# Optimization experiments

Measured on AMD Instinct MI355X. Metric: run time of the kernel, lower is better.

The kernel has to match this reference:

```python
import jax, jax.numpy as jnp
import numpy as np

N, E = 40000, 640000
D, H, DK = 128, 8, 16   # out_dim, n_heads, d_k = D // H
T, R = 3, 4             # num node types, num relation types


def setup_inputs() -> dict:
    key = jax.random.key(0)
    ks = jax.random.split(key, 16)
    glorot = lambda k, shape, fan: jax.random.normal(k, shape, jnp.float32) * np.sqrt(2.0 / fan)
    inp = {
        'node_inp': jax.random.normal(ks[0], (N, D), jnp.float32),
        'node_type': jax.random.randint(ks[1], (N,), 0, T),
        'edge_index': jax.random.randint(ks[2], (2, E), 0, N),
        'edge_type': jax.random.randint(ks[3], (E,), 0, R),
        'node_position': jax.random.randint(ks[4], (N,), 0, N),
        # per-node-type Linear weights, stored [T, in, out] (y = x @ W + b)
        'Kw': glorot(ks[5], (T, D, D), 2 * D), 'Kb': jnp.zeros((T, D), jnp.float32),
        'Qw': glorot(ks[6], (T, D, D), 2 * D), 'Qb': jnp.zeros((T, D), jnp.float32),
        'Vw': glorot(ks[7], (T, D, D), 2 * D), 'Vb': jnp.zeros((T, D), jnp.float32),
        'Aw': glorot(ks[8], (T, D, D), 2 * D), 'Ab': jnp.zeros((T, D), jnp.float32),
        'relation_pri': jnp.ones((T, R, T, H), jnp.float32),
        'relation_att': glorot(ks[9], (R, H, DK, DK), 2 * DK),
        'relation_msg': glorot(ks[10], (R, H, DK, DK), 2 * DK),
        'relation_s2u': glorot(ks[11], (D, D), 2 * D),
        'skip': jnp.ones((T,), jnp.float32),
    }
    return inp


def reference(node_inp, node_type, edge_index, edge_type, node_position,
              Kw, Kb, Qw, Qb, Vw, Vb, Aw, Ab,
              relation_pri, relation_att, relation_msg, relation_s2u, skip):
    n = node_inp.shape[0]
    src, tgt = edge_index[0], edge_index[1]  # j (source), i (target)
    ar = jnp.arange(n)

    # per-type K/Q/V projections for every node: [T, N, D], then select own type
    k_all = jnp.einsum('nd,tdo->tno', node_inp, Kw) + Kb[:, None, :]
    q_all = jnp.einsum('nd,tdo->tno', node_inp, Qw) + Qb[:, None, :]
    v_all = jnp.einsum('nd,tdo->tno', node_inp, Vw) + Vb[:, None, :]
    k_node = k_all[node_type, ar]
    q_node = q_all[node_type, ar]
    v_node = v_all[node_type, ar]

    k_j = k_node[src].reshape(-1, H, DK)
    v_j = v_node[src].reshape(-1, H, DK)
    q_i = q_node[tgt].reshape(-1, H, DK)

    # per-relation attention / message transforms (select per edge relation)
    k_t = jnp.zeros_like(k_j)
    v_t = jnp.zeros_like(v_j)
    for r in range(R):
        sel = (edge_type == r)[:, None, None]
        k_t = jnp.where(sel, jnp.einsum('ehd,hdf->ehf', k_j, relation_att[r]), k_t)
        v_t = jnp.where(sel, jnp.einsum('ehd,hdf->ehf', v_j, relation_msg[r]), v_t)

    st, tt = node_type[src], node_type[tgt]
    pri = relation_pri[tt, edge_type, st]                       # [E, H]
    att_raw = (q_i * k_t).sum(-1) * pri / np.sqrt(DK)           # [E, H]

    # scatter-softmax over edges sharing the same target node
    m = jax.ops.segment_max(att_raw, tgt, num_segments=n)
    m = jnp.where(jnp.isfinite(m), m, 0.0)
    ex = jnp.exp(att_raw - m[tgt])
    den = jax.ops.segment_sum(ex, tgt, num_segments=n)
    att = ex / (den[tgt] + 1e-16)

    msg = (v_t * att[:, :, None]).reshape(-1, D)
    aggr = jax.ops.segment_sum(msg, tgt, num_segments=n)        # scatter-add

    # speaker information: edges with edge_type==0, message from target rep to source index
    sp_in = v_all[1][tgt]                                       # v_linears[1](node_inp[edge_index_i])
    sp_msg = sp_in @ relation_s2u                               # [E, D]
    drop_idx = jnp.where(edge_type == 0, src, n)                # out-of-range -> dropped
    speaker_info = jnp.zeros((n, D), node_inp.dtype).at[drop_idx].set(sp_msg, mode='drop')

    aggr = jax.nn.gelu(aggr + speaker_info, approximate=False)

    # target-specific aggregation with per-type learnable skip (dropout=eval identity)
    a_all = jnp.einsum('no,tof->tnf', aggr, Aw) + Ab[:, None, :]
    a_node = a_all[node_type, ar]
    alpha = jax.nn.sigmoid(skip)[node_type][:, None]
    return a_node * alpha + node_inp * (1.0 - alpha)
```

## Files before the change

### kernel.cpp

```cpp
#include <hip/hip_runtime.h>
#include <hip/hip_bf16.h>
#include <math.h>

#define ND 128
#define NH 8
#define DKK 16
#define NT 3
#define NR 4
#define NB 8
#define NMAT 12
#define SCB 4096

typedef unsigned short ushort_t;
typedef __bf16 bf16_t;
typedef bf16_t bf16x8 __attribute__((ext_vector_type(8)));
typedef float f32x4 __attribute__((ext_vector_type(4)));

__device__ __forceinline__ float bf2f(unsigned short u) {
    union { unsigned int i; float f; } v; v.i = ((unsigned int)u) << 16; return v.f;
}
__device__ __forceinline__ unsigned short f2bf(float f) {
    union { float f; unsigned int i; } v; v.f = f;
    unsigned int x = v.i;
    unsigned int lsb = (x >> 16) & 1u;
    x += 0x7fffu + lsb;
    return (unsigned short)(x >> 16);
}
__device__ __forceinline__ unsigned int pk2(float a, float b) {
    return (unsigned int)f2bf(a) | ((unsigned int)f2bf(b) << 16);
}
__device__ __forceinline__ void load_bf8(const ushort_t* p, float* o) {
    uint4 u = *reinterpret_cast<const uint4*>(p);
    o[0]=bf2f(u.x & 0xffff); o[1]=bf2f(u.x >> 16);
    o[2]=bf2f(u.y & 0xffff); o[3]=bf2f(u.y >> 16);
    o[4]=bf2f(u.z & 0xffff); o[5]=bf2f(u.z >> 16);
    o[6]=bf2f(u.w & 0xffff); o[7]=bf2f(u.w >> 16);
}
__device__ __forceinline__ bf16x8 as_bf16x8(uint4 u) {
    union { uint4 u; bf16x8 v; } c; c.u = u; return c.v;
}


__global__ void k_zero(int n, int* offs, int* winner, int* tcnt) {
    int i = blockIdx.x * 256 + threadIdx.x;
    if (i < n) { offs[i] = 0; winner[i] = -1; }
    if (i < NT) tcnt[i] = 0;
}

__global__ void k_count(int n, int e, const int* src, const int* tgt, const int* etype,
                        const int* ntype, int* offs, int* winner, int* tcnt, int* rank) {
    int i = blockIdx.x * 256 + threadIdx.x;
    if (i < e) {
        rank[i] = atomicAdd(&offs[tgt[i]], 1);
        if (etype[i] == 0) atomicMax(&winner[src[i]], i);
    }
    if (i < n) {
        int t = ntype[i];
        int lane = threadIdx.x & 63;
        #pragma unroll
        for (int tt = 0; tt < NT; tt++) {
            bool me = (t == tt);
            unsigned long long m = __ballot(me);
            if (me) {
                int lower = __popcll(m & ((1ull << lane) - 1ull));
                if (lower == 0) atomicAdd(&tcnt[tt], __popcll(m));
            }
        }
    }
}


__global__ void k_scanA(int n, const int* offs, int* bsum) {
    __shared__ int red[256];
    int b = blockIdx.x, tid = threadIdx.x;
    int base = b * SCB + tid * 16;
    int s = 0;
    #pragma unroll
    for (int i = 0; i < 16; i++) {
        int idx = base + i;
        if (idx < n) s += offs[idx];
    }
    red[tid] = s;
    __syncthreads();
    for (int d = 128; d > 0; d >>= 1) {
        if (tid < d) red[tid] += red[tid + d];
        __syncthreads();
    }
    if (tid == 0) bsum[b] = red[0];
}

__global__ void k_scanB(int nb, const int* bsum, int* boff,
                        const int* tcnt, int* tnext, int* tstart) {
    if (threadIdx.x == 0) {
        int run = 0;
        for (int b = 0; b < nb; b++) { boff[b] = run; run += bsum[b]; }
        int t0 = 0;
        for (int t = 0; t < NT; t++) { tnext[t] = t0; tstart[t] = t0; t0 += tcnt[t]; }
    }
}

__global__ void k_scanC(int n, int* offs, const int* boff) {
    __shared__ int red[256];
    int b = blockIdx.x, tid = threadIdx.x;
    int base = b * SCB + tid * 16;
    int v[16];
    int s = 0;
    #pragma unroll
    for (int i = 0; i < 16; i++) {
        int idx = base + i;
        v[i] = (idx < n) ? offs[idx] : 0;
        s += v[i];
    }
    red[tid] = s;
    __syncthreads();
    for (int d = 1; d < 256; d <<= 1) {
        int vv = (tid >= d) ? red[tid - d] : 0;
        __syncthreads();
        red[tid] += vv;
        __syncthreads();
    }
    int run = boff[b] + red[tid] - s;
    #pragma unroll
    for (int i = 0; i < 16; i++) {
        int idx = base + i;
        if (idx < n) { offs[idx] = run; run += v[i]; }
    }
    if (base <= n && n < base + 16) offs[n] = run;
}

__global__ void k_scatter(int n, int e, const int* src, const int* tgt, const int* etype,
                          const int* ntype, const int* offs, const int* rank,
                          int* eord, int mode, int* tnext, int* order) {
    int i = blockIdx.x * 256 + threadIdx.x;
    if (i < e) {
        int p = offs[tgt[i]] + rank[i];
        if (mode) {
            int s = src[i];
            eord[p] = (s * NR + etype[i]) | (ntype[s] << 28);
        } else {
            eord[p] = i;
        }
    }
    if (i < n) {
        int t = ntype[i];
        int lane = threadIdx.x & 63;
        #pragma unroll
        for (int tt = 0; tt < NT; tt++) {
            bool me = (t == tt);
            unsigned long long m = __ballot(me);
            if (me) {
                int lower = __popcll(m & ((1ull << lane) - 1ull));
                int leader = __ffsll((long long)m) - 1;
                int base = 0;
                if (lane == leader) base = atomicAdd(&tnext[tt], __popcll(m));
                base = __shfl(base, leader, 64);
                order[base + lower] = i;
            }
        }
    }
}


__global__ void k_pack(const float* Qw, const float* Qb, const float* Kw, const float* Kb,
                       const float* Vw, const float* Vb, const float* Aw, const float* Ab,
                       const float* s2u, const float* r_att, const float* r_msg,
                       ushort_t* Wall, float* bcat) {
    int blk = blockIdx.x;
    int kb = blk & 3;
    int c = (blk >> 2) & 7;
    int tm = blk >> 5;
    int m = tm % NMAT, t = tm / NMAT;
    int lane = threadIdx.x;
    int nn = c * 16 + (lane & 15);
    int quad = lane >> 4;
    int k0 = kb * 32 + quad * 8;
    ushort_t* dst = Wall + (size_t)blk * 512 + lane * 8;

    if (m == 0 || m == 5 || m == 10 || m == 11) {
        const float* W; const float* B;
        if (m == 0)       { W = Qw + (size_t)t * ND * ND; B = Qb + t * ND; }
        else if (m == 5)  { W = Vw + (size_t)ND * ND;     B = Vb + ND; }
        else if (m == 10) { W = Aw + (size_t)t * ND * ND; B = Ab + t * ND; }
        else              { W = s2u;                      B = nullptr; }
        #pragma unroll
        for (int j = 0; j < 8; j++) dst[j] = f2bf(W[(size_t)(k0 + j) * ND + nn]);
        if (kb == 0 && quad == 0)
            bcat[(t * NMAT + m) * ND + nn] = B ? B[nn] : 0.f;
    } else {
        int r = (m <= 4) ? (m - 1) : (m - 6);
        const float* W0 = (m <= 4) ? Kw : Vw;
        const float* B0 = (m <= 4) ? Kb : Vb;
        const float* Wr = (m <= 4) ? r_att : r_msg;
        int h = c, f = lane & 15;
        float wcol[16];
        #pragma unroll
        for (int jj = 0; jj < 16; jj++)
            wcol[jj] = Wr[(((size_t)r * NH + h) * DKK + jj) * DKK + f];
        #pragma unroll
        for (int j = 0; j < 8; j++) {
            const float* row = W0 + ((size_t)t * ND + (k0 + j)) * ND + h * DKK;
            float s = 0.f;
            #pragma unroll
            for (int jj = 0; jj < 16; jj++) s += row[jj] * wcol[jj];
            dst[j] = f2bf(s);
        }
        if (kb == 0 && quad == 0) {
            const float* brow = B0 + t * ND + h * DKK;
            float sb = 0.f;
            #pragma unroll
            for (int jj = 0; jj < 16; jj++) sb += brow[jj] * wcol[jj];
            bcat[(t * NMAT + m) * ND + nn] = sb;
        }
    }
}

__global__ void __launch_bounds__(256) k_projm(
    int n, const float* x_in, const int* order,
    const int* tcnt, const int* tstart,
    const ushort_t* Wall, const float* bcat,
    int m0, int nm,
    ushort_t* out_qn, ushort_t* out_kt, ushort_t* out_v1, ushort_t* out_vt)
{
    __shared__ __align__(16) ushort_t xs[4096];
    __shared__ int nodes[32];
    int b = blockIdx.x;
    int nb0 = (tcnt[0] + 31) >> 5, nb1 = (tcnt[1] + 31) >> 5, nb2 = (tcnt[2] + 31) >> 5;
    int t, lb;
    if (b < nb0)                  { t = 0; lb = b; }
    else if (b < nb0 + nb1)       { t = 1; lb = b - nb0; }
    else if (b < nb0 + nb1 + nb2) { t = 2; lb = b - nb0 - nb1; }
    else return;
    int segoff = lb * 32;
    int cnt = min(32, tcnt[t] - segoff);
    int segbase = tstart[t] + segoff;
    int tid = threadIdx.x;
    if (tid < 32) nodes[tid] = (tid < cnt) ? order[segbase + tid] : -1;
    __syncthreads();
    {
        int row = tid >> 3;
        int d0 = (tid & 7) * 16;
        int rt = row >> 4, rl = row & 15;
        int kb = d0 >> 5, q0 = (d0 >> 3) & 3;
        uint4 c0, c1;
        if (row < cnt) {
            const float4* xp4 = (const float4*)(x_in + (size_t)nodes[row] * ND + d0);
            float4 a = xp4[0], b2 = xp4[1], c2 = xp4[2], d4 = xp4[3];
            c0.x = pk2(a.x, a.y);   c0.y = pk2(a.z, a.w);
            c0.z = pk2(b2.x, b2.y); c0.w = pk2(b2.z, b2.w);
            c1.x = pk2(c2.x, c2.y); c1.y = pk2(c2.z, c2.w);
            c1.z = pk2(d4.x, d4.y); c1.w = pk2(d4.z, d4.w);
        } else {
            c0.x = c0.y = c0.z = c0.w = 0u;
            c1 = c0;
        }
        *(uint4*)&xs[((rt * 4 + kb) * 64 + q0 * 16 + rl) * 8]       = c0;
        *(uint4*)&xs[((rt * 4 + kb) * 64 + (q0 + 1) * 16 + rl) * 8] = c1;
    }
    __syncthreads();

    int w = tid >> 6, lane = tid & 63;
    int rt = w & 1;
    bf16x8 afr[4];
    #pragma unroll
    for (int kb = 0; kb < 4; kb++)
        afr[kb] = as_bf16x8(*(const uint4*)&xs[((rt * 4 + kb) * 64 + lane) * 8]);
    int nct = nm * 8;
    for (int ct = (w >> 1); ct < nct; ct += 2) {
        int m = m0 + (ct >> 3), c = ct & 7;
        const uint4* bp = (const uint4*)(Wall + ((((size_t)t * NMAT + m) * 8 + c) * 4) * 512);
        f32x4 acc = {0.f, 0.f, 0.f, 0.f};
        #pragma unroll
        for (int kb = 0; kb < 4; kb++) {
            bf16x8 bfr = as_bf16x8(bp[kb * 64 + lane]);
            acc = __builtin_amdgcn_mfma_f32_16x16x32_bf16(afr[kb], bfr, acc, 0, 0, 0);
        }
        int col = c * 16 + (lane & 15);
        float bias = bcat[(t * NMAT + m) * ND + col];
        int rbase = rt * 16 + (lane >> 4) * 4;
        #pragma unroll
        for (int r = 0; r < 4; r++) {
            int grow = rbase + r;
            if (grow >= cnt) continue;
            int node = nodes[grow];
            ushort_t val = f2bf(acc[r] + bias);
            if (m == 0)       out_qn[(size_t)node * ND + col] = val;
            else if (m <= 4)  out_kt[((size_t)node * NR + (m - 1)) * ND + col] = val;
            else if (m == 5)  out_v1[(size_t)node * ND + col] = val;
            else              out_vt[((size_t)node * NR + (m - 6)) * ND + col] = val;
        }
    }
}

__global__ void __launch_bounds__(256) k_sfinal(
    int n, const float* x_in, const int* order, const int* tcnt, const int* tstart,
    const int* winner, const int* tgt, const ushort_t* v1b,
    const ushort_t* Wall, const float* bcat, const float* skip,
    const float* aggr, float* out)
{
    __shared__ __align__(16) float xf[32 * 132];
    __shared__ __align__(16) ushort_t xs[4096];
    __shared__ int nodes[32];
    __shared__ int wsrc[32];
    int b = blockIdx.x;
    int nb0 = (tcnt[0] + 31) >> 5, nb1 = (tcnt[1] + 31) >> 5, nb2 = (tcnt[2] + 31) >> 5;
    int t, lb;
    if (b < nb0)                  { t = 0; lb = b; }
    else if (b < nb0 + nb1)       { t = 1; lb = b - nb0; }
    else if (b < nb0 + nb1 + nb2) { t = 2; lb = b - nb0 - nb1; }
    else return;
    int segoff = lb * 32;
    int cnt = min(32, tcnt[t] - segoff);
    int segbase = tstart[t] + segoff;
    int tid = threadIdx.x;
    if (tid < 32) {
        int nd = (tid < cnt) ? order[segbase + tid] : -1;
        nodes[tid] = nd;
        int wi = (nd >= 0) ? winner[nd] : -1;
        wsrc[tid] = (wi >= 0) ? tgt[wi] : -1;
    }
    __syncthreads();
    {
        int row = tid >> 3;
        int d0 = (tid & 7) * 16;
        int rt = row >> 4, rl = row & 15;
        int kb = d0 >> 5, q0 = (d0 >> 3) & 3;
        uint4 c0, c1;
        int s = (row < cnt) ? wsrc[row] : -1;
        if (s >= 0) {
            const uint4* vp = (const uint4*)(v1b + (size_t)s * ND + d0);
            c0 = vp[0]; c1 = vp[1];
        } else { c0.x = c0.y = c0.z = c0.w = 0u; c1 = c0; }
        *(uint4*)&xs[((rt * 4 + kb) * 64 + q0 * 16 + rl) * 8]       = c0;
        *(uint4*)&xs[((rt * 4 + kb) * 64 + (q0 + 1) * 16 + rl) * 8] = c1;
    }
    __syncthreads();
    int w = tid >> 6, lane = tid & 63;
    int rt = w & 1;
    {
        bf16x8 afr[4];
        #pragma unroll
        for (int kb = 0; kb < 4; kb++)
            afr[kb] = as_bf16x8(*(const uint4*)&xs[((rt * 4 + kb) * 64 + lane) * 8]);
        for (int ct = (w >> 1); ct < 8; ct += 2) {
            const uint4* bp = (const uint4*)(Wall + (((size_t)11 * 8 + ct) * 4) * 512);
            f32x4 acc = {0.f, 0.f, 0.f, 0.f};
            #pragma unroll
            for (int kb = 0; kb < 4; kb++) {
                bf16x8 bfr = as_bf16x8(bp[kb * 64 + lane]);
                acc = __builtin_amdgcn_mfma_f32_16x16x32_bf16(afr[kb], bfr, acc, 0, 0, 0);
            }
            int col = ct * 16 + (lane & 15);
            int rbase = rt * 16 + (lane >> 4) * 4;
            #pragma unroll
            for (int r = 0; r < 4; r++) {
                int grow = rbase + r;
                if (grow >= cnt) continue;
                int node = nodes[grow];
                float g = aggr[(size_t)node * ND + col] + acc[r];
                g = 0.5f * g * (1.f + erff(g * 0.70710678118f));
                xf[grow * 132 + col] = g;
            }
        }
    }
    __syncthreads();
    {
        int row = tid >> 3;
        int d0 = (tid & 7) * 16;
        int rt2 = row >> 4, rl = row & 15;
        int kb = d0 >> 5, q0 = (d0 >> 3) & 3;
        uint4 c0, c1;
        if (row < cnt) {
            const float4* xp4 = (const float4*)(xf + row * 132 + d0);
            float4 a = xp4[0], b2 = xp4[1], c2 = xp4[2], d4 = xp4[3];
            c0.x = pk2(a.x, a.y);   c0.y = pk2(a.z, a.w);
            c0.z = pk2(b2.x, b2.y); c0.w = pk2(b2.z, b2.w);
            c1.x = pk2(c2.x, c2.y); c1.y = pk2(c2.z, c2.w);
            c1.z = pk2(d4.x, d4.y); c1.w = pk2(d4.z, d4.w);
        } else {
            c0.x = c0.y = c0.z = c0.w = 0u;
            c1 = c0;
        }
        *(uint4*)&xs[((rt2 * 4 + kb) * 64 + q0 * 16 + rl) * 8]       = c0;
        *(uint4*)&xs[((rt2 * 4 + kb) * 64 + (q0 + 1) * 16 + rl) * 8] = c1;
    }
    __syncthreads();
    float alpha = 1.f / (1.f + expf(-skip[t]));
    {
        bf16x8 afr[4];
        #pragma unroll
        for (int kb = 0; kb < 4; kb++)
            afr[kb] = as_bf16x8(*(const uint4*)&xs[((rt * 4 + kb) * 64 + lane) * 8]);
        for (int ct = (w >> 1); ct < 8; ct += 2) {
            const uint4* bp = (const uint4*)(Wall + ((((size_t)t * NMAT + 10) * 8 + ct) * 4) * 512);
            f32x4 acc = {0.f, 0.f, 0.f, 0.f};
            #pragma unroll
            for (int kb = 0; kb < 4; kb++) {
                bf16x8 bfr = as_bf16x8(bp[kb * 64 + lane]);
                acc = __builtin_amdgcn_mfma_f32_16x16x32_bf16(afr[kb], bfr, acc, 0, 0, 0);
            }
            int col = ct * 16 + (lane & 15);
            float bias = bcat[(t * NMAT + 10) * ND + col];
            int rbase = rt * 16 + (lane >> 4) * 4;
            #pragma unroll
            for (int r = 0; r < 4; r++) {
                int grow = rbase + r;
                if (grow >= cnt) continue;
                int node = nodes[grow];
                float xin = x_in[(size_t)node * ND + col];
                out[(size_t)node * ND + col] = (acc[r] + bias) * alpha + xin * (1.f - alpha);
            }
        }
    }
}

__global__ void __launch_bounds__(256) k_attmd(
    int n, const int* off, const int* srp, const int* ntype,
    const ushort_t* qn, const ushort_t* kt, const float* r_pri,
    float* atts, ushort_t* mb, float* db)
{
    int wv = threadIdx.x >> 6, lane = threadIdx.x & 63;
    int i = blockIdx.x * 4 + wv;
    if (i >= n) return;
    int h = lane & 7, slot = lane >> 3;
    int tt = ntype[i];
    float qf[16];
    load_bf8(qn + (size_t)i * ND + h * DKK, qf);
    load_bf8(qn + (size_t)i * ND + h * DKK + 8, qf + 8);
    const float* prib = r_pri + (size_t)(tt * NR * NT) * NH + h;
    int d0 = off[i], d1 = off[i + 1];
    float m = -3.0e38f, den = 0.f;
    #pragma unroll 2
    for (int p0 = d0; p0 < d1; p0 += 8) {
        int p = p0 + slot;
        bool live = (p < d1);
        int sp = live ? srp[p] : 0;
        int sr = sp & 0x0fffffff;
        int st = ((unsigned int)sp) >> 28;
        int r = sr & (NR - 1);
        float kf[16];
        const ushort_t* kp = kt + (size_t)sr * ND + h * DKK;
        load_bf8(kp, kf);
        load_bf8(kp + 8, kf + 8);
        float a = 0.f;
        #pragma unroll
        for (int f = 0; f < 16; f++) a += qf[f] * kf[f];
        float pri = prib[(r * NT + st) * NH];
        float logit = fminf(fmaxf(a * pri * 0.25f, -1.0e4f), 1.0e4f);
        if (live) {
            atts[(size_t)p * NH + h] = logit;
            float mnew = fmaxf(m, logit);
            den = den * expf(m - mnew) + expf(logit - mnew);
            m = mnew;
        }
    }
    #pragma unroll
    for (int d = 8; d < 64; d <<= 1) {
        float mo = __shfl_xor(m, d, 64);
        float dn = __shfl_xor(den, d, 64);
        float mnew = fmaxf(m, mo);
        den = den * expf(m - mnew) + dn * expf(mo - mnew);
        m = mnew;
    }
    if (slot == 0) {
        ushort_t mh = (d1 > d0) ? f2bf(m) : (ushort_t)0;
        float dfin = (d1 > d0) ? den * expf(m - bf2f(mh)) : 0.f;
        mb[i * NH + h] = mh;
        db[i * NH + h] = dfin;
    }
}

__global__ void __launch_bounds__(256) k_aggr_fast(
    int n, const int* off, const int* srp, const ushort_t* vt, const float* atts,
    const ushort_t* mb, const float* db, float* aggr)
{
    int wv = threadIdx.x >> 6, lane = threadIdx.x & 63;
    int i = blockIdx.x * 4 + wv;
    if (i >= n) return;
    int h = lane >> 3;
    float mref = bf2f(mb[i * NH + h]);
    float inv = 1.f / (db[i * NH + h] + 1e-16f);
    int d0 = off[i], d1 = off[i + 1];
    float acc0 = 0.f, acc1 = 0.f;
    #pragma unroll 4
    for (int p = d0; p < d1; p++) {
        int sr = srp[p] & 0x0fffffff;
        float w = expf(atts[(size_t)p * NH + h] - mref) * inv;
        unsigned int u = *reinterpret_cast<const unsigned int*>(
            vt + (size_t)sr * ND + lane * 2);
        acc0 += w * bf2f(u & 0xffff);
        acc1 += w * bf2f(u >> 16);
    }
    float2 o; o.x = acc0; o.y = acc1;
    *reinterpret_cast<float2*>(aggr + (size_t)i * ND + lane * 2) = o;
}


__global__ void k_proj(int n, const float* x_in, const int* ntype, const int* order,
                       const float* Kw, const float* Kb,
                       const float* Qw, const float* Qb,
                       const float* Vw, const float* Vb,
                       ushort_t* kn, ushort_t* qn, ushort_t* vn, ushort_t* v1) {
    __shared__ float xs[NB][ND];
    __shared__ int nodes[NB];
    __shared__ int types[NB];
    int tid = threadIdx.x;
    int base = blockIdx.x * NB;
    int cnt = min(NB, n - base);
    if (tid < cnt) { int nd = order[base + tid]; nodes[tid] = nd; types[tid] = ntype[nd]; }
    __syncthreads();
    for (int j = 0; j < cnt; j++) xs[j][tid] = x_in[(size_t)nodes[j] * ND + tid];
    __syncthreads();
    bool uni = (types[0] == types[cnt - 1]);
    for (int m = 0; m < 4; m++) {
        const float *W, *B; ushort_t* out; int forced_t = -1;
        if (m == 0)      { W = Kw; B = Kb; out = kn; }
        else if (m == 1) { W = Qw; B = Qb; out = qn; }
        else if (m == 2) { W = Vw; B = Vb; out = vn; }
        else             { W = Vw; B = Vb; out = v1; forced_t = 1; }
        if (uni || forced_t >= 0) {
            int t = (forced_t >= 0) ? forced_t : types[0];
            float bias = B[t * ND + tid];
            float acc[NB];
            #pragma unroll
            for (int j = 0; j < NB; j++) acc[j] = bias;
            const float* Wp = W + (size_t)t * ND * ND + tid;
            for (int d = 0; d < ND; d++) {
                float w = Wp[(size_t)d * ND];
                #pragma unroll
                for (int j = 0; j < NB; j++) acc[j] += xs[j][d] * w;
            }
            for (int j = 0; j < cnt; j++) out[(size_t)nodes[j] * ND + tid] = f2bf(acc[j]);
        } else {
            for (int j = 0; j < cnt; j++) {
                int t = types[j];
                float acc = B[t * ND + tid];
                const float* Wp = W + (size_t)t * ND * ND + tid;
                for (int d = 0; d < ND; d++) acc += xs[j][d] * Wp[(size_t)d * ND];
                out[(size_t)nodes[j] * ND + tid] = f2bf(acc);
            }
        }
    }
}

__global__ void k_att(int e, const int* src, const int* tgt, const int* etype, const int* ntype,
                      const ushort_t* kn, const ushort_t* qn,
                      const float* r_att, const float* r_pri, float* att) {
    int id = blockIdx.x * 256 + threadIdx.x;
    if (id >= e * NH) return;
    int ee = id >> 3, h = id & 7;
    int s = src[ee], t = tgt[ee], r = etype[ee];
    float kf[16], qf[16];
    load_bf8(kn + (size_t)s * ND + h * DKK, kf);
    load_bf8(kn + (size_t)s * ND + h * DKK + 8, kf + 8);
    load_bf8(qn + (size_t)t * ND + h * DKK, qf);
    load_bf8(qn + (size_t)t * ND + h * DKK + 8, qf + 8);
    const float* W = r_att + (size_t)(r * NH + h) * DKK * DKK;
    float kt[16];
    #pragma unroll
    for (int f = 0; f < 16; f++) kt[f] = 0.f;
    #pragma unroll 4
    for (int d = 0; d < 16; d++) {
        float kd = kf[d];
        #pragma unroll
        for (int f = 0; f < 16; f++) kt[f] += kd * W[d * 16 + f];
    }
    float a = 0.f;
    #pragma unroll
    for (int f = 0; f < 16; f++) a += qf[f] * kt[f];
    int tt = ntype[t], st = ntype[s];
    float pri = r_pri[((tt * NR + r) * NT + st) * NH + h];
    float logit = a * pri * 0.25f;
    logit = fminf(fmaxf(logit, -1.0e4f), 1.0e4f);
    att[(size_t)ee * NH + h] = logit;
}

__global__ void k_mden(int n, const int* off, const int* sorted,
                       const float* att, ushort_t* mb, float* db) {
    int id = blockIdx.x * 256 + threadIdx.x;
    if (id >= n * NH) return;
    int i = id >> 3, h = id & 7;
    int d0 = off[i], d1 = off[i + 1];
    float m = -3.0e38f;
    for (int p = d0; p < d1; p++) m = fmaxf(m, att[(size_t)sorted[p] * NH + h]);
    ushort_t mh = (d1 > d0) ? f2bf(m) : (ushort_t)0;
    float mref = bf2f(mh);
    float den = 0.f;
    for (int p = d0; p < d1; p++) den += expf(att[(size_t)sorted[p] * NH + h] - mref);
    mb[id] = mh;
    db[id] = den;
}

__global__ void k_norm(int e, const int* tgt, const ushort_t* mb, const float* db, float* att) {
    int id = blockIdx.x * 256 + threadIdx.x;
    if (id >= e * NH) return;
    int ee = id >> 3, h = id & 7;
    int t = tgt[ee];
    float w = expf(att[id] - bf2f(mb[t * NH + h])) / (db[t * NH + h] + 1e-16f);
    att[id] = w;
}

__global__ void k_aggr(int n, const int* off, const int* sorted, const int* src, const int* etype,
                       const ushort_t* vn, const float* r_msg, const float* att, float* aggr) {
    int wv = threadIdx.x >> 6, lane = threadIdx.x & 63;
    int i = blockIdx.x * 4 + wv;
    if (i >= n) return;
    int h = lane >> 3, f0 = (lane & 7) * 2;
    int d0 = off[i], d1 = off[i + 1];
    float acc0 = 0.f, acc1 = 0.f;
    for (int p = d0; p < d1; p++) {
        int ee = sorted[p];
        int s = src[ee], r = etype[ee];
        float w = att[(size_t)ee * NH + h];
        float vj[16];
        load_bf8(vn + (size_t)s * ND + h * DKK, vj);
        load_bf8(vn + (size_t)s * ND + h * DKK + 8, vj + 8);
        const float* Wm = r_msg + (size_t)(r * NH + h) * DKK * DKK + f0;
        float a0 = 0.f, a1 = 0.f;
        #pragma unroll
        for (int d = 0; d < 16; d++) {
            a0 += vj[d] * Wm[d * 16];
            a1 += vj[d] * Wm[d * 16 + 1];
        }
        acc0 += w * a0; acc1 += w * a1;
    }
    aggr[(size_t)i * ND + h * DKK + f0]     = acc0;
    aggr[(size_t)i * ND + h * DKK + f0 + 1] = acc1;
}

__global__ void k_spk(int n, const int* winner, const int* tgt, const ushort_t* v1,
                      const float* s2u, float* aggr) {
    __shared__ float xs[NB][ND];
    __shared__ int wn[NB];
    int tid = threadIdx.x;
    int base = blockIdx.x * NB;
    int cnt = min(NB, n - base);
    if (tid < cnt) wn[tid] = winner[base + tid];
    __syncthreads();
    for (int j = 0; j < cnt; j++) {
        int w = wn[j];
        xs[j][tid] = (w >= 0) ? bf2f(v1[(size_t)tgt[w] * ND + tid]) : 0.f;
    }
    __syncthreads();
    float acc[NB];
    #pragma unroll
    for (int j = 0; j < NB; j++) acc[j] = 0.f;
    const float* Wp = s2u + tid;
    for (int d = 0; d < ND; d++) {
        float w = Wp[(size_t)d * ND];
        #pragma unroll
        for (int j = 0; j < NB; j++) acc[j] += xs[j][d] * w;
    }
    for (int j = 0; j < cnt; j++) {
        size_t idx = (size_t)(base + j) * ND + tid;
        float g = aggr[idx] + acc[j];
        g = 0.5f * g * (1.f + erff(g * 0.70710678118f));
        aggr[idx] = g;
    }
}

__global__ void k_final(int n, const float* x_in, const int* ntype, const int* order,
                        const float* Aw, const float* Ab, const float* skip,
                        const float* aggr, float* out) {
    __shared__ float xs[NB][ND];
    __shared__ int nodes[NB];
    __shared__ int types[NB];
    int tid = threadIdx.x;
    int base = blockIdx.x * NB;
    int cnt = min(NB, n - base);
    if (tid < cnt) { int nd = order[base + tid]; nodes[tid] = nd; types[tid] = ntype[nd]; }
    __syncthreads();
    for (int j = 0; j < cnt; j++) xs[j][tid] = aggr[(size_t)nodes[j] * ND + tid];
    __syncthreads();
    bool uni = (types[0] == types[cnt - 1]);
    if (uni) {
        int t = types[0];
        float bias = Ab[t * ND + tid];
        float acc[NB];
        #pragma unroll
        for (int j = 0; j < NB; j++) acc[j] = bias;
        const float* Wp = Aw + (size_t)t * ND * ND + tid;
        for (int d = 0; d < ND; d++) {
            float w = Wp[(size_t)d * ND];
            #pragma unroll
            for (int j = 0; j < NB; j++) acc[j] += xs[j][d] * w;
        }
        float alpha = 1.f / (1.f + expf(-skip[t]));
        for (int j = 0; j < cnt; j++) {
            float xin = x_in[(size_t)nodes[j] * ND + tid];
            out[(size_t)nodes[j] * ND + tid] = acc[j] * alpha + xin * (1.f - alpha);
        }
    } else {
        for (int j = 0; j < cnt; j++) {
            int t = types[j];
            float acc = Ab[t * ND + tid];
            const float* Wp = Aw + (size_t)t * ND * ND + tid;
            for (int d = 0; d < ND; d++) acc += xs[j][d] * Wp[(size_t)d * ND];
            float alpha = 1.f / (1.f + expf(-skip[t]));
            float xin = x_in[(size_t)nodes[j] * ND + tid];
            out[(size_t)nodes[j] * ND + tid] = acc * alpha + xin * (1.f - alpha);
        }
    }
}

extern "C" void kernel_launch(void* const* d_in, const int* in_sizes, int n_in,
                              void* d_out, int out_size, void* d_ws, size_t ws_size,
                              hipStream_t stream) {
    const float* node_inp = (const float*)d_in[0];
    const int* node_type  = (const int*)d_in[1];
    const int* edge_index = (const int*)d_in[2];
    const int* edge_type  = (const int*)d_in[3];
    const float* Kw = (const float*)d_in[5];
    const float* Kb = (const float*)d_in[6];
    const float* Qw = (const float*)d_in[7];
    const float* Qb = (const float*)d_in[8];
    const float* Vw = (const float*)d_in[9];
    const float* Vb = (const float*)d_in[10];
    const float* Aw = (const float*)d_in[11];
    const float* Ab = (const float*)d_in[12];
    const float* r_pri = (const float*)d_in[13];
    const float* r_att = (const float*)d_in[14];
    const float* r_msg = (const float*)d_in[15];
    const float* s2u   = (const float*)d_in[16];
    const float* skip  = (const float*)d_in[17];

    int n = in_sizes[1];
    int e = in_sizes[3];
    const int* srcp = edge_index;
    const int* tgtp = edge_index + e;

    char* wsp = (char*)d_ws;
    size_t woff = 0;
    auto alloc = [&](size_t b) { void* p = wsp + woff; woff += (b + 255) & ~(size_t)255; return p; };

    int* offs     = (int*)alloc((size_t)(n + 1) * 4);
    int* winner   = (int*)alloc((size_t)n * 4);
    int* order    = (int*)alloc((size_t)n * 4);
    int* tcnt     = (int*)alloc(16);
    int* tnext    = (int*)alloc(16);
    int* tstart   = (int*)alloc(16);
    int* bsum     = (int*)alloc(4096);
    int* boff     = (int*)alloc(4096);
    int* eord     = (int*)alloc((size_t)e * 4);
    ushort_t* mb  = (ushort_t*)alloc((size_t)n * NH * 2);
    float* db     = (float*)alloc((size_t)n * NH * 4);
    ushort_t* v1b = (ushort_t*)alloc((size_t)n * ND * 2);
    float* att    = (float*)alloc((size_t)e * NH * 4);
    size_t commonEnd = woff;

    int* rank = (int*)att;

    ushort_t* Wall  = (ushort_t*)alloc((size_t)NT * NMAT * 8 * 4 * 512 * 2);
    float* bcat     = (float*)alloc((size_t)NT * NMAT * ND * 4);
    char* F         = (char*)alloc((size_t)n * 1536);
    size_t fastEnd = woff;

    int gn = (n + 255) / 256;
    int ge = (e + 255) / 256;
    int nbscan = n / SCB + 1;
    int fast = (ws_size >= fastEnd) ? 1 : 0;

    k_zero<<<gn, 256, 0, stream>>>(n, offs, winner, tcnt);
    k_count<<<ge, 256, 0, stream>>>(n, e, srcp, tgtp, edge_type, node_type, offs, winner, tcnt, rank);
    k_scanA<<<nbscan, 256, 0, stream>>>(n, offs, bsum);
    k_scanB<<<1, 64, 0, stream>>>(nbscan, bsum, boff, tcnt, tnext, tstart);
    k_scanC<<<nbscan, 256, 0, stream>>>(n, offs, boff);
    k_scatter<<<ge, 256, 0, stream>>>(n, e, srcp, tgtp, edge_type, node_type, offs, rank,
                                      eord, fast, tnext, order);

    if (fast) {
        ushort_t* qn  = (ushort_t*)F;
        ushort_t* kt  = (ushort_t*)(F + (size_t)n * 256);
        ushort_t* vt  = (ushort_t*)F;
        float* aggr   = (float*)(F + (size_t)n * 1024);
        int gproj = (n + 31) / 32 + NT;

        k_pack<<<NT * NMAT * 8 * 4, 64, 0, stream>>>(Qw, Qb, Kw, Kb, Vw, Vb, Aw, Ab,
                                                     s2u, r_att, r_msg, Wall, bcat);
        k_projm<<<gproj, 256, 0, stream>>>(n, node_inp, order, tcnt, tstart, Wall, bcat,
                                           0, 6, qn, kt, v1b, (ushort_t*)nullptr);
        k_attmd<<<(n + 3) / 4, 256, 0, stream>>>(n, offs, eord, node_type,
                                                 qn, kt, r_pri, att, mb, db);
        k_projm<<<gproj, 256, 0, stream>>>(n, node_inp, order, tcnt, tstart, Wall, bcat,
                                           6, 4, (ushort_t*)nullptr, (ushort_t*)nullptr,
                                           (ushort_t*)nullptr, vt);
        k_aggr_fast<<<(n + 3) / 4, 256, 0, stream>>>(n, offs, eord, vt, att, mb, db, aggr);
        k_sfinal<<<gproj, 256, 0, stream>>>(n, node_inp, order, tcnt, tstart,
                                            winner, tgtp, v1b, Wall, bcat, skip,
                                            aggr, (float*)d_out);
    } else {
        woff = commonEnd;
        ushort_t* vn  = (ushort_t*)alloc((size_t)n * ND * 2);
        char* regA    = (char*)alloc((size_t)n * ND * 2 * 2);
        ushort_t* kn  = (ushort_t*)regA;
        ushort_t* qn  = (ushort_t*)(regA + (size_t)n * ND * 2);
        float* aggr   = (float*)regA;

        k_proj<<<(n + NB - 1) / NB, 128, 0, stream>>>(n, node_inp, node_type, order,
                                                      Kw, Kb, Qw, Qb, Vw, Vb, kn, qn, vn, v1b);
        k_att<<<(e * NH + 255) / 256, 256, 0, stream>>>(e, srcp, tgtp, edge_type, node_type,
                                                        kn, qn, r_att, r_pri, att);
        k_mden<<<(n * NH + 255) / 256, 256, 0, stream>>>(n, offs, eord, att, mb, db);
        k_norm<<<(e * NH + 255) / 256, 256, 0, stream>>>(e, tgtp, mb, db, att);
        k_aggr<<<(n + 3) / 4, 256, 0, stream>>>(n, offs, eord, srcp, edge_type, vn, r_msg, att, aggr);
        k_spk<<<(n + NB - 1) / NB, 128, 0, stream>>>(n, winner, tgtp, v1b, s2u, aggr);
        k_final<<<(n + NB - 1) / NB, 128, 0, stream>>>(n, node_inp, node_type, order,
                                                       Aw, Ab, skip, aggr, (float*)d_out);
    }
}
```

Before: 352.9 us.

## Fuse edge counting with first projection kernel and split node-type ordering

```diff
diff --git a/kernel.cpp b/kernel.cpp
--- a/kernel.cpp
+++ b/kernel.cpp
@@ -41,20 +41,14 @@
 }
 
 
-__global__ void k_zero(int n, int* offs, int* winner, int* tcnt) {
+__global__ void k_z6(int* tcnt) {
+    if (threadIdx.x < 8) tcnt[threadIdx.x] = 0;
+}
+
+__global__ void k_zinit(int n, int* offs, int* winner, const int* ntype, int* tcnt) {
     int i = blockIdx.x * 256 + threadIdx.x;
-    if (i < n) { offs[i] = 0; winner[i] = -1; }
-    if (i < NT) tcnt[i] = 0;
-}
-
-__global__ void k_count(int n, int e, const int* src, const int* tgt, const int* etype,
-                        const int* ntype, int* offs, int* winner, int* tcnt, int* rank) {
-    int i = blockIdx.x * 256 + threadIdx.x;
-    if (i < e) {
-        rank[i] = atomicAdd(&offs[tgt[i]], 1);
-        if (etype[i] == 0) atomicMax(&winner[src[i]], i);
-    }
     if (i < n) {
+        offs[i] = 0; winner[i] = -1;
         int t = ntype[i];
         int lane = threadIdx.x & 63;
         #pragma unroll
@@ -66,6 +60,38 @@
                 if (lower == 0) atomicAdd(&tcnt[tt], __popcll(m));
             }
         }
+    }
+}
+
+__global__ void k_nscatter(int n, const int* ntype, const int* tcnt, int* tpos, int* order) {
+    int i = blockIdx.x * 256 + threadIdx.x;
+    if (i < n) {
+        int tc0 = tcnt[0], tc1 = tcnt[1];
+        int t = ntype[i];
+        int lane = threadIdx.x & 63;
+        #pragma unroll
+        for (int tt = 0; tt < NT; tt++) {
+            bool me = (t == tt);
+            unsigned long long m = __ballot(me);
+            if (me) {
+                int ts = (tt == 0) ? 0 : ((tt == 1) ? tc0 : tc0 + tc1);
+                int lower = __popcll(m & ((1ull << lane) - 1ull));
+                int leader = __ffsll((long long)m) - 1;
+                int base = 0;
+                if (lane == leader) base = atomicAdd(&tpos[tt], __popcll(m));
+                base = __shfl(base, leader, 64);
+                order[ts + base + lower] = i;
+            }
+        }
+    }
+}
+
+__global__ void k_count_e(int e, const int* src, const int* tgt, const int* etype,
+                          int* offs, int* winner, int* rank) {
+    int i = blockIdx.x * 256 + threadIdx.x;
+    if (i < e) {
+        rank[i] = atomicAdd(&offs[tgt[i]], 1);
+        if (etype[i] == 0) atomicMax(&winner[src[i]], i);
     }
 }
 
@@ -89,13 +115,10 @@
     if (tid == 0) bsum[b] = red[0];
 }
 
-__global__ void k_scanB(int nb, const int* bsum, int* boff,
-                        const int* tcnt, int* tnext, int* tstart) {
+__global__ void k_scanB(int nb, const int* bsum, int* boff) {
     if (threadIdx.x == 0) {
         int run = 0;
         for (int b = 0; b < nb; b++) { boff[b] = run; run += bsum[b]; }
-        int t0 = 0;
-        for (int t = 0; t < NT; t++) { tnext[t] = t0; tstart[t] = t0; t0 += tcnt[t]; }
     }
 }
 
@@ -128,9 +151,9 @@
     if (base <= n && n < base + 16) offs[n] = run;
 }
 
-__global__ void k_scatter(int n, int e, const int* src, const int* tgt, const int* etype,
-                          const int* ntype, const int* offs, const int* rank,
-                          int* eord, int mode, int* tnext, int* order) {
+__global__ void k_scatter_e(int e, const int* src, const int* tgt, const int* etype,
+                            const int* ntype, const int* offs, const int* rank,
+                            int* eord, int mode) {
     int i = blockIdx.x * 256 + threadIdx.x;
     if (i < e) {
         int p = offs[tgt[i]] + rank[i];
@@ -139,23 +162,6 @@
             eord[p] = (s * NR + etype[i]) | (ntype[s] << 28);
         } else {
             eord[p] = i;
-        }
-    }
-    if (i < n) {
-        int t = ntype[i];
-        int lane = threadIdx.x & 63;
-        #pragma unroll
-        for (int tt = 0; tt < NT; tt++) {
-            bool me = (t == tt);
-            unsigned long long m = __ballot(me);
-            if (me) {
-                int lower = __popcll(m & ((1ull << lane) - 1ull));
-                int leader = __ffsll((long long)m) - 1;
-                int base = 0;
-                if (lane == leader) base = atomicAdd(&tnext[tt], __popcll(m));
-                base = __shfl(base, leader, 64);
-                order[base + lower] = i;
-            }
         }
     }
 }
@@ -214,25 +220,35 @@
     }
 }
 
-__global__ void __launch_bounds__(256) k_projm(
-    int n, const float* x_in, const int* order,
-    const int* tcnt, const int* tstart,
+__global__ void __launch_bounds__(256) k_fuse1(
+    int n, int e, int ge, const int* src, const int* tgt, const int* etype,
+    int* offs, int* winner, int* rank,
+    const float* x_in, const int* order, const int* tcnt,
     const ushort_t* Wall, const float* bcat,
-    int m0, int nm,
-    ushort_t* out_qn, ushort_t* out_kt, ushort_t* out_v1, ushort_t* out_vt)
+    ushort_t* out_qn, ushort_t* out_kt, ushort_t* out_v1)
 {
     __shared__ __align__(16) ushort_t xs[4096];
     __shared__ int nodes[32];
-    int b = blockIdx.x;
-    int nb0 = (tcnt[0] + 31) >> 5, nb1 = (tcnt[1] + 31) >> 5, nb2 = (tcnt[2] + 31) >> 5;
-    int t, lb;
-    if (b < nb0)                  { t = 0; lb = b; }
-    else if (b < nb0 + nb1)       { t = 1; lb = b - nb0; }
-    else if (b < nb0 + nb1 + nb2) { t = 2; lb = b - nb0 - nb1; }
+    int bb = blockIdx.x;
+    if (bb < ge) {
+        int i = bb * 256 + threadIdx.x;
+        if (i < e) {
+            rank[i] = atomicAdd(&offs[tgt[i]], 1);
+            if (etype[i] == 0) atomicMax(&winner[src[i]], i);
+        }
+        return;
+    }
+    int b = bb - ge;
+    int c0t = tcnt[0], c1t = tcnt[1], c2t = tcnt[2];
+    int nb0 = (c0t + 31) >> 5, nb1 = (c1t + 31) >> 5, nb2 = (c2t + 31) >> 5;
+    int t, lb, ts, tct;
+    if (b < nb0)                  { t = 0; lb = b;             ts = 0;         tct = c0t; }
+    else if (b < nb0 + nb1)       { t = 1; lb = b - nb0;       ts = c0t;       tct = c1t; }
+    else if (b < nb0 + nb1 + nb2) { t = 2; lb = b - nb0 - nb1; ts = c0t + c1t; tct = c2t; }
     else return;
     int segoff = lb * 32;
-    int cnt = min(32, tcnt[t] - segoff);
-    int segbase = tstart[t] + segoff;
+    int cnt = min(32, tct - segoff);
+    int segbase = ts + segoff;
     int tid = threadIdx.x;
     if (tid < 32) nodes[tid] = (tid < cnt) ? order[segbase + tid] : -1;
     __syncthreads();
@@ -264,9 +280,8 @@
     #pragma unroll
     for (int kb = 0; kb < 4; kb++)
         afr[kb] = as_bf16x8(*(const uint4*)&xs[((rt * 4 + kb) * 64 + lane) * 8]);
-    int nct = nm * 8;
-    for (int ct = (w >> 1); ct < nct; ct += 2) {
-        int m = m0 + (ct >> 3), c = ct & 7;
+    for (int ct = (w >> 1); ct < 48; ct += 2) {
+        int m = ct >> 3, c = ct & 7;
         const uint4* bp = (const uint4*)(Wall + ((((size_t)t * NMAT + m) * 8 + c) * 4) * 512);
         f32x4 acc = {0.f, 0.f, 0.f, 0.f};
         #pragma unroll
@@ -285,14 +300,84 @@
             ushort_t val = f2bf(acc[r] + bias);
             if (m == 0)       out_qn[(size_t)node * ND + col] = val;
             else if (m <= 4)  out_kt[((size_t)node * NR + (m - 1)) * ND + col] = val;
-            else if (m == 5)  out_v1[(size_t)node * ND + col] = val;
-            else              out_vt[((size_t)node * NR + (m - 6)) * ND + col] = val;
+            else              out_v1[(size_t)node * ND + col] = val;
+        }
+    }
+}
+
+__global__ void __launch_bounds__(256) k_projm(
+    int n, const float* x_in, const int* order, const int* tcnt,
+    const ushort_t* Wall, const float* bcat,
+    ushort_t* out_vt)
+{
+    __shared__ __align__(16) ushort_t xs[4096];
+    __shared__ int nodes[32];
+    int b = blockIdx.x;
+    int c0t = tcnt[0], c1t = tcnt[1], c2t = tcnt[2];
+    int nb0 = (c0t + 31) >> 5, nb1 = (c1t + 31) >> 5, nb2 = (c2t + 31) >> 5;
+    int t, lb, ts, tct;
+    if (b < nb0)                  { t = 0; lb = b;             ts = 0;         tct = c0t; }
+    else if (b < nb0 + nb1)       { t = 1; lb = b - nb0;       ts = c0t;       tct = c1t; }
+    else if (b < nb0 + nb1 + nb2) { t = 2; lb = b - nb0 - nb1; ts = c0t + c1t; tct = c2t; }
+    else return;
+    int segoff = lb * 32;
+    int cnt = min(32, tct - segoff);
+    int segbase = ts + segoff;
+    int tid = threadIdx.x;
+    if (tid < 32) nodes[tid] = (tid < cnt) ? order[segbase + tid] : -1;
+    __syncthreads();
+    {
+        int row = tid >> 3;
+        int d0 = (tid & 7) * 16;
+        int rt = row >> 4, rl = row & 15;
+        int kb = d0 >> 5, q0 = (d0 >> 3) & 3;
+        uint4 c0, c1;
+        if (row < cnt) {
+            const float4* xp4 = (const float4*)(x_in + (size_t)nodes[row] * ND + d0);
+            float4 a = xp4[0], b2 = xp4[1], c2 = xp4[2], d4 = xp4[3];
+            c0.x = pk2(a.x, a.y);   c0.y = pk2(a.z, a.w);
+            c0.z = pk2(b2.x, b2.y); c0.w = pk2(b2.z, b2.w);
+            c1.x = pk2(c2.x, c2.y); c1.y = pk2(c2.z, c2.w);
+            c1.z = pk2(d4.x, d4.y); c1.w = pk2(d4.z, d4.w);
+        } else {
+            c0.x = c0.y = c0.z = c0.w = 0u;
+            c1 = c0;
+        }
+        *(uint4*)&xs[((rt * 4 + kb) * 64 + q0 * 16 + rl) * 8]       = c0;
+        *(uint4*)&xs[((rt * 4 + kb) * 64 + (q0 + 1) * 16 + rl) * 8] = c1;
+    }
+    __syncthreads();
+
+    int w = tid >> 6, lane = tid & 63;
+    int rt = w & 1;
+    bf16x8 afr[4];
+    #pragma unroll
+    for (int kb = 0; kb < 4; kb++)
+        afr[kb] = as_bf16x8(*(const uint4*)&xs[((rt * 4 + kb) * 64 + lane) * 8]);
+    for (int ct = (w >> 1); ct < 32; ct += 2) {
+        int m = 6 + (ct >> 3), c = ct & 7;
+        const uint4* bp = (const uint4*)(Wall + ((((size_t)t * NMAT + m) * 8 + c) * 4) * 512);
+        f32x4 acc = {0.f, 0.f, 0.f, 0.f};
+        #pragma unroll
+        for (int kb = 0; kb < 4; kb++) {
+            bf16x8 bfr = as_bf16x8(bp[kb * 64 + lane]);
+            acc = __builtin_amdgcn_mfma_f32_16x16x32_bf16(afr[kb], bfr, acc, 0, 0, 0);
+        }
+        int col = c * 16 + (lane & 15);
+        float bias = bcat[(t * NMAT + m) * ND + col];
+        int rbase = rt * 16 + (lane >> 4) * 4;
+        #pragma unroll
+        for (int r = 0; r < 4; r++) {
+            int grow = rbase + r;
+            if (grow >= cnt) continue;
+            int node = nodes[grow];
+            out_vt[((size_t)node * NR + (m - 6)) * ND + col] = f2bf(acc[r] + bias);
         }
     }
 }
 
 __global__ void __launch_bounds__(256) k_sfinal(
-    int n, const float* x_in, const int* order, const int* tcnt, const int* tstart,
+    int n, const float* x_in, const int* order, const int* tcnt,
     const int* winner, const int* tgt, const ushort_t* v1b,
     const ushort_t* Wall, const float* bcat, const float* skip,
     const float* aggr, float* out)
@@ -302,15 +387,16 @@
     __shared__ int nodes[32];
     __shared__ int wsrc[32];
     int b = blockIdx.x;
-    int nb0 = (tcnt[0] + 31) >> 5, nb1 = (tcnt[1] + 31) >> 5, nb2 = (tcnt[2] + 31) >> 5;
-    int t, lb;
-    if (b < nb0)                  { t = 0; lb = b; }
-    else if (b < nb0 + nb1)       { t = 1; lb = b - nb0; }
-    else if (b < nb0 + nb1 + nb2) { t = 2; lb = b - nb0 - nb1; }
+    int c0t = tcnt[0], c1t = tcnt[1], c2t = tcnt[2];
+    int nb0 = (c0t + 31) >> 5, nb1 = (c1t + 31) >> 5, nb2 = (c2t + 31) >> 5;
+    int t, lb, ts, tct;
+    if (b < nb0)                  { t = 0; lb = b;             ts = 0;         tct = c0t; }
+    else if (b < nb0 + nb1)       { t = 1; lb = b - nb0;       ts = c0t;       tct = c1t; }
+    else if (b < nb0 + nb1 + nb2) { t = 2; lb = b - nb0 - nb1; ts = c0t + c1t; tct = c2t; }
     else return;
     int segoff = lb * 32;
-    int cnt = min(32, tcnt[t] - segoff);
-    int segbase = tstart[t] + segoff;
+    int cnt = min(32, tct - segoff);
+    int segbase = ts + segoff;
     int tid = threadIdx.x;
     if (tid < 32) {
         int nd = (tid < cnt) ? order[segbase + tid] : -1;
@@ -735,9 +821,8 @@
     int* offs     = (int*)alloc((size_t)(n + 1) * 4);
     int* winner   = (int*)alloc((size_t)n * 4);
     int* order    = (int*)alloc((size_t)n * 4);
-    int* tcnt     = (int*)alloc(16);
-    int* tnext    = (int*)alloc(16);
-    int* tstart   = (int*)alloc(16);
+    int* tcnt     = (int*)alloc(32);
+    int* tpos     = tcnt + 4;
     int* bsum     = (int*)alloc(4096);
     int* boff     = (int*)alloc(4096);
     int* eord     = (int*)alloc((size_t)e * 4);
@@ -759,13 +844,9 @@
     int nbscan = n / SCB + 1;
     int fast = (ws_size >= fastEnd) ? 1 : 0;
 
-    k_zero<<<gn, 256, 0, stream>>>(n, offs, winner, tcnt);
-    k_count<<<ge, 256, 0, stream>>>(n, e, srcp, tgtp, edge_type, node_type, offs, winner, tcnt, rank);
-    k_scanA<<<nbscan, 256, 0, stream>>>(n, offs, bsum);
-    k_scanB<<<1, 64, 0, stream>>>(nbscan, bsum, boff, tcnt, tnext, tstart);
-    k_scanC<<<nbscan, 256, 0, stream>>>(n, offs, boff);
-    k_scatter<<<ge, 256, 0, stream>>>(n, e, srcp, tgtp, edge_type, node_type, offs, rank,
-                                      eord, fast, tnext, order);
+    k_z6<<<1, 64, 0, stream>>>(tcnt);
+    k_zinit<<<gn, 256, 0, stream>>>(n, offs, winner, node_type, tcnt);
+    k_nscatter<<<gn, 256, 0, stream>>>(n, node_type, tcnt, tpos, order);
 
     if (fast) {
         ushort_t* qn  = (ushort_t*)F;
@@ -776,15 +857,20 @@
 
         k_pack<<<NT * NMAT * 8 * 4, 64, 0, stream>>>(Qw, Qb, Kw, Kb, Vw, Vb, Aw, Ab,
                                                      s2u, r_att, r_msg, Wall, bcat);
-        k_projm<<<gproj, 256, 0, stream>>>(n, node_inp, order, tcnt, tstart, Wall, bcat,
-                                           0, 6, qn, kt, v1b, (ushort_t*)nullptr);
+        k_fuse1<<<ge + gproj, 256, 0, stream>>>(n, e, ge, srcp, tgtp, edge_type,
+                                                offs, winner, rank,
+                                                node_inp, order, tcnt, Wall, bcat,
+                                                qn, kt, v1b);
+        k_scanA<<<nbscan, 256, 0, stream>>>(n, offs, bsum);
+        k_scanB<<<1, 64, 0, stream>>>(nbscan, bsum, boff);
+        k_scanC<<<nbscan, 256, 0, stream>>>(n, offs, boff);
+        k_scatter_e<<<ge, 256, 0, stream>>>(e, srcp, tgtp, edge_type, node_type,
+                                            offs, rank, eord, 1);
         k_attmd<<<(n + 3) / 4, 256, 0, stream>>>(n, offs, eord, node_type,
                                                  qn, kt, r_pri, att, mb, db);
-        k_projm<<<gproj, 256, 0, stream>>>(n, node_inp, order, tcnt, tstart, Wall, bcat,
-                                           6, 4, (ushort_t*)nullptr, (ushort_t*)nullptr,
-                                           (ushort_t*)nullptr, vt);
+        k_projm<<<gproj, 256, 0, stream>>>(n, node_inp, order, tcnt, Wall, bcat, vt);
         k_aggr_fast<<<(n + 3) / 4, 256, 0, stream>>>(n, offs, eord, vt, att, mb, db, aggr);
-        k_sfinal<<<gproj, 256, 0, stream>>>(n, node_inp, order, tcnt, tstart,
+        k_sfinal<<<gproj, 256, 0, stream>>>(n, node_inp, order, tcnt,
                                             winner, tgtp, v1b, Wall, bcat, skip,
                                             aggr, (float*)d_out);
     } else {
@@ -795,6 +881,12 @@
         ushort_t* qn  = (ushort_t*)(regA + (size_t)n * ND * 2);
         float* aggr   = (float*)regA;
 
+        k_count_e<<<ge, 256, 0, stream>>>(e, srcp, tgtp, edge_type, offs, winner, rank);
+        k_scanA<<<nbscan, 256, 0, stream>>>(n, offs, bsum);
+        k_scanB<<<1, 64, 0, stream>>>(nbscan, bsum, boff);
+        k_scanC<<<nbscan, 256, 0, stream>>>(n, offs, boff);
+        k_scatter_e<<<ge, 256, 0, stream>>>(e, srcp, tgtp, edge_type, node_type,
+                                            offs, rank, eord, 0);
         k_proj<<<(n + NB - 1) / NB, 128, 0, stream>>>(n, node_inp, node_type, order,
                                                       Kw, Kb, Qw, Qb, Vw, Vb, kn, qn, vn, v1b);
         k_att<<<(e * NH + 255) / 256, 256, 0, stream>>>(e, srcp, tgtp, edge_type, node_type,
```

Result: slower. 369.6 us (+4.7%).

## Fuse attention softmax and aggregation into single online-softmax flash kernel

Applied to the files above, without the earlier changes.

```diff
diff --git a/kernel.cpp b/kernel.cpp
--- a/kernel.cpp
+++ b/kernel.cpp
@@ -289,6 +289,148 @@
             else              out_vt[((size_t)node * NR + (m - 6)) * ND + col] = val;
         }
     }
+}
+
+__global__ void __launch_bounds__(256) k_projall(
+    int n, const float* x_in, const int* order,
+    const int* tcnt, const int* tstart,
+    const ushort_t* Wall, const float* bcat,
+    ushort_t* out_qn, ushort_t* out_kt, ushort_t* out_v1, ushort_t* out_vt)
+{
+    __shared__ __align__(16) ushort_t xs[4096];
+    __shared__ int nodes[32];
+    int b = blockIdx.x;
+    int nb0 = (tcnt[0] + 31) >> 5, nb1 = (tcnt[1] + 31) >> 5, nb2 = (tcnt[2] + 31) >> 5;
+    int t, lb;
+    if (b < nb0)                  { t = 0; lb = b; }
+    else if (b < nb0 + nb1)       { t = 1; lb = b - nb0; }
+    else if (b < nb0 + nb1 + nb2) { t = 2; lb = b - nb0 - nb1; }
+    else return;
+    int segoff = lb * 32;
+    int cnt = min(32, tcnt[t] - segoff);
+    int segbase = tstart[t] + segoff;
+    int tid = threadIdx.x;
+    if (tid < 32) nodes[tid] = (tid < cnt) ? order[segbase + tid] : -1;
+    __syncthreads();
+    {
+        int row = tid >> 3;
+        int d0 = (tid & 7) * 16;
+        int rt = row >> 4, rl = row & 15;
+        int kb = d0 >> 5, q0 = (d0 >> 3) & 3;
+        uint4 c0, c1;
+        if (row < cnt) {
+            const float4* xp4 = (const float4*)(x_in + (size_t)nodes[row] * ND + d0);
+            float4 a = xp4[0], b2 = xp4[1], c2 = xp4[2], d4 = xp4[3];
+            c0.x = pk2(a.x, a.y);   c0.y = pk2(a.z, a.w);
+            c0.z = pk2(b2.x, b2.y); c0.w = pk2(b2.z, b2.w);
+            c1.x = pk2(c2.x, c2.y); c1.y = pk2(c2.z, c2.w);
+            c1.z = pk2(d4.x, d4.y); c1.w = pk2(d4.z, d4.w);
+        } else {
+            c0.x = c0.y = c0.z = c0.w = 0u;
+            c1 = c0;
+        }
+        *(uint4*)&xs[((rt * 4 + kb) * 64 + q0 * 16 + rl) * 8]       = c0;
+        *(uint4*)&xs[((rt * 4 + kb) * 64 + (q0 + 1) * 16 + rl) * 8] = c1;
+    }
+    __syncthreads();
+
+    int w = tid >> 6, lane = tid & 63;
+    int rt = w & 1;
+    bf16x8 afr[4];
+    #pragma unroll
+    for (int kb = 0; kb < 4; kb++)
+        afr[kb] = as_bf16x8(*(const uint4*)&xs[((rt * 4 + kb) * 64 + lane) * 8]);
+    for (int ct = (w >> 1); ct < 80; ct += 2) {
+        int m = ct >> 3, c = ct & 7;
+        const uint4* bp = (const uint4*)(Wall + ((((size_t)t * NMAT + m) * 8 + c) * 4) * 512);
+        f32x4 acc = {0.f, 0.f, 0.f, 0.f};
+        #pragma unroll
+        for (int kb = 0; kb < 4; kb++) {
+            bf16x8 bfr = as_bf16x8(bp[kb * 64 + lane]);
+            acc = __builtin_amdgcn_mfma_f32_16x16x32_bf16(afr[kb], bfr, acc, 0, 0, 0);
+        }
+        int col = c * 16 + (lane & 15);
+        float bias = bcat[(t * NMAT + m) * ND + col];
+        int rbase = rt * 16 + (lane >> 4) * 4;
+        #pragma unroll
+        for (int r = 0; r < 4; r++) {
+            int grow = rbase + r;
+            if (grow >= cnt) continue;
+            int node = nodes[grow];
+            ushort_t val = f2bf(acc[r] + bias);
+            if (m == 0)       out_qn[(size_t)node * ND + col] = val;
+            else if (m <= 4)  out_kt[((size_t)node * NR + (m - 1)) * ND + col] = val;
+            else if (m == 5)  out_v1[(size_t)node * ND + col] = val;
+            else              out_vt[((size_t)node * NR + (m - 6)) * ND + col] = val;
+        }
+    }
+}
+
+__global__ void __launch_bounds__(256) k_flash(
+    int n, const int* off, const int* srp, const int* ntype,
+    const ushort_t* qn, const ushort_t* kt, const ushort_t* vt,
+    const float* r_pri, float* aggr)
+{
+    int wv = threadIdx.x >> 6, lane = threadIdx.x & 63;
+    int i = blockIdx.x * 4 + wv;
+    if (i >= n) return;
+    int h = lane & 7, slot = lane >> 3;
+    int hA = lane >> 3;
+    int tt = ntype[i];
+    float qf[16];
+    load_bf8(qn + (size_t)i * ND + h * DKK, qf);
+    load_bf8(qn + (size_t)i * ND + h * DKK + 8, qf + 8);
+    const float* prib = r_pri + (size_t)(tt * NR * NT) * NH + h;
+    int d0 = off[i], d1 = off[i + 1];
+    float m = -3.0e38f, den = 0.f;
+    float acc0 = 0.f, acc1 = 0.f;
+    for (int p0 = d0; p0 < d1; p0 += 8) {
+        int p = p0 + slot;
+        bool live = (p < d1);
+        int sp = live ? srp[p] : 0;
+        int sr = sp & 0x0fffffff;
+        int st = ((unsigned int)sp) >> 28;
+        int r = sr & (NR - 1);
+        float kf[16];
+        const ushort_t* kp = kt + (size_t)sr * ND + h * DKK;
+        load_bf8(kp, kf);
+        load_bf8(kp + 8, kf + 8);
+        float a = 0.f;
+        #pragma unroll
+        for (int f = 0; f < 16; f++) a += qf[f] * kf[f];
+        float pri = prib[(r * NT + st) * NH];
+        float logit = fminf(fmaxf(a * pri * 0.25f, -1.0e4f), 1.0e4f);
+        if (!live) logit = -3.0e38f;
+        float cm = logit;
+        #pragma unroll
+        for (int d = 8; d < 64; d <<= 1) cm = fmaxf(cm, __shfl_xor(cm, d, 64));
+        float mnew = fmaxf(m, cm);
+        float w = live ? expf(logit - mnew) : 0.f;
+        float ws = w;
+        #pragma unroll
+        for (int d = 8; d < 64; d <<= 1) ws += __shfl_xor(ws, d, 64);
+        float scale = expf(m - mnew);
+        den = den * scale + ws;
+        m = mnew;
+        float scaleA = __shfl(scale, hA, 64);
+        acc0 *= scaleA; acc1 *= scaleA;
+        #pragma unroll
+        for (int s = 0; s < 8; s++) {
+            if (p0 + s < d1) {
+                int srcl = s * 8 + hA;
+                int srb  = __shfl(sr, srcl, 64);
+                float wb = __shfl(w, srcl, 64);
+                unsigned int u = *reinterpret_cast<const unsigned int*>(
+                    vt + (size_t)srb * ND + lane * 2);
+                acc0 += wb * bf2f(u & 0xffff);
+                acc1 += wb * bf2f(u >> 16);
+            }
+        }
+    }
+    float denA = __shfl(den, hA, 64);
+    float inv = 1.f / (denA + 1e-16f);
+    float2 o; o.x = acc0 * inv; o.y = acc1 * inv;
+    *reinterpret_cast<float2*>(aggr + (size_t)i * ND + lane * 2) = o;
 }
 
 __global__ void __launch_bounds__(256) k_sfinal(
@@ -749,15 +891,28 @@
 
     int* rank = (int*)att;
 
-    ushort_t* Wall  = (ushort_t*)alloc((size_t)NT * NMAT * 8 * 4 * 512 * 2);
-    float* bcat     = (float*)alloc((size_t)NT * NMAT * ND * 4);
+    woff = commonEnd;
+    ushort_t* WallB = (ushort_t*)alloc((size_t)NT * NMAT * 8 * 4 * 512 * 2);
+    float* bcatB    = (float*)alloc((size_t)NT * NMAT * ND * 4);
     char* F         = (char*)alloc((size_t)n * 1536);
     size_t fastEnd = woff;
+
+    woff = commonEnd;
+    ushort_t* WallA = (ushort_t*)alloc((size_t)NT * NMAT * 8 * 4 * 512 * 2);
+    float* bcatA    = (float*)alloc((size_t)NT * NMAT * ND * 4);
+    ushort_t* qnA   = (ushort_t*)alloc((size_t)n * ND * 2);
+    ushort_t* ktA   = (ushort_t*)alloc((size_t)n * NR * ND * 2);
+    ushort_t* vtA   = (ushort_t*)alloc((size_t)n * NR * ND * 2);
+    size_t tierAEnd = woff;
+    float* aggrA = (float*)att;
 
     int gn = (n + 255) / 256;
     int ge = (e + 255) / 256;
     int nbscan = n / SCB + 1;
-    int fast = (ws_size >= fastEnd) ? 1 : 0;
+    int gproj = (n + 31) / 32 + NT;
+
+    int tierA = (ws_size >= tierAEnd) && ((size_t)e * NH >= (size_t)n * ND);
+    int fast  = (ws_size >= fastEnd);
 
     k_zero<<<gn, 256, 0, stream>>>(n, offs, winner, tcnt);
     k_count<<<ge, 256, 0, stream>>>(n, e, srcp, tgtp, edge_type, node_type, offs, winner, tcnt, rank);
@@ -765,27 +920,36 @@
     k_scanB<<<1, 64, 0, stream>>>(nbscan, bsum, boff, tcnt, tnext, tstart);
     k_scanC<<<nbscan, 256, 0, stream>>>(n, offs, boff);
     k_scatter<<<ge, 256, 0, stream>>>(n, e, srcp, tgtp, edge_type, node_type, offs, rank,
-                                      eord, fast, tnext, order);
-
-    if (fast) {
+                                      eord, (tierA || fast) ? 1 : 0, tnext, order);
+
+    if (tierA) {
+        k_pack<<<NT * NMAT * 8 * 4, 64, 0, stream>>>(Qw, Qb, Kw, Kb, Vw, Vb, Aw, Ab,
+                                                     s2u, r_att, r_msg, WallA, bcatA);
+        k_projall<<<gproj, 256, 0, stream>>>(n, node_inp, order, tcnt, tstart, WallA, bcatA,
+                                             qnA, ktA, v1b, vtA);
+        k_flash<<<(n + 3) / 4, 256, 0, stream>>>(n, offs, eord, node_type,
+                                                 qnA, ktA, vtA, r_pri, aggrA);
+        k_sfinal<<<gproj, 256, 0, stream>>>(n, node_inp, order, tcnt, tstart,
+                                            winner, tgtp, v1b, WallA, bcatA, skip,
+                                            aggrA, (float*)d_out);
+    } else if (fast) {
         ushort_t* qn  = (ushort_t*)F;
         ushort_t* kt  = (ushort_t*)(F + (size_t)n * 256);
         ushort_t* vt  = (ushort_t*)F;
         float* aggr   = (float*)(F + (size_t)n * 1024);
-        int gproj = (n + 31) / 32 + NT;
 
         k_pack<<<NT * NMAT * 8 * 4, 64, 0, stream>>>(Qw, Qb, Kw, Kb, Vw, Vb, Aw, Ab,
-                                                     s2u, r_att, r_msg, Wall, bcat);
-        k_projm<<<gproj, 256, 0, stream>>>(n, node_inp, order, tcnt, tstart, Wall, bcat,
+                                                     s2u, r_att, r_msg, WallB, bcatB);
+        k_projm<<<gproj, 256, 0, stream>>>(n, node_inp, order, tcnt, tstart, WallB, bcatB,
                                            0, 6, qn, kt, v1b, (ushort_t*)nullptr);
         k_attmd<<<(n + 3) / 4, 256, 0, stream>>>(n, offs, eord, node_type,
                                                  qn, kt, r_pri, att, mb, db);
-        k_projm<<<gproj, 256, 0, stream>>>(n, node_inp, order, tcnt, tstart, Wall, bcat,
+        k_projm<<<gproj, 256, 0, stream>>>(n, node_inp, order, tcnt, tstart, WallB, bcatB,
                                            6, 4, (ushort_t*)nullptr, (ushort_t*)nullptr,
                                            (ushort_t*)nullptr, vt);
         k_aggr_fast<<<(n + 3) / 4, 256, 0, stream>>>(n, offs, eord, vt, att, mb, db, aggr);
         k_sfinal<<<gproj, 256, 0, stream>>>(n, node_inp, order, tcnt, tstart,
-                                            winner, tgtp, v1b, Wall, bcat, skip,
+                                            winner, tgtp, v1b, WallB, bcatB, skip,
                                             aggr, (float*)d_out);
     } else {
         woff = commonEnd;
```

Measured after the change: 350.1 us. About the same (-0.8%).
